# Kernel optimization log

Measured on AMD Instinct MI355X. Metric: run time of the kernel, lower is better.

Reference implementation:

```python
import jax, jax.numpy as jnp
import numpy as np

KERNEL_SIZE = 32
STRIDE = 16


def _block_compress(x, w, pe):
    # x: [B, N, H, D]; w: [K]; pe: [K, D]
    B, N, H, D = x.shape
    M = (N - KERNEL_SIZE) // STRIDE + 1
    # window gather indices: [M, K]
    idx = jnp.arange(M)[:, None] * STRIDE + jnp.arange(KERNEL_SIZE)[None, :]
    xw = x[:, idx]  # [B, M, K, H, D]
    # y = sum_k w[k] * (x_window + pe) / kernel_size
    return jnp.einsum('bmkhd,k->bmhd', xw + pe[None, None, :, None, :], w) / KERNEL_SIZE


def setup_inputs() -> dict:
    key = jax.random.key(0)
    k1, k2, k3, k4, k5, k6, k7 = jax.random.split(key, 7)
    B, N, QH, KH, D, VD = 1, 8192, 32, 2, 128, 128
    return {
        'q': jax.random.normal(k1, (B, N, QH, D), dtype=jnp.float32),
        'k': jax.random.normal(k2, (B, N, KH, D), dtype=jnp.float32),
        'v': jax.random.normal(k3, (B, N, KH, VD), dtype=jnp.float32),
        'w_key': jax.random.normal(k4, (KERNEL_SIZE,), dtype=jnp.float32),
        'pe_key': jax.random.normal(k5, (KERNEL_SIZE, D), dtype=jnp.float32),
        'w_val': jax.random.normal(k6, (KERNEL_SIZE,), dtype=jnp.float32),
        'pe_val': jax.random.normal(k7, (KERNEL_SIZE, VD), dtype=jnp.float32),
    }


def reference(q, k, v, w_key, pe_key, w_val, pe_val):
    ck = _block_compress(k, w_key, pe_key)  # [B, M, KH, D]
    cv = _block_compress(v, w_val, pe_val)  # [B, M, KH, VD]
    B, N, QH, D = q.shape
    M, KH = ck.shape[1], ck.shape[2]
    G = QH // KH  # GQA group size; off_kh = off_qh // G -> qh index = kh*G + g
    sm_scale = D ** -0.5
    qg = q.reshape(B, N, KH, G, D)
    # scores: [B, KH, G, N, M]
    scores = jnp.einsum('bnhgd,bmhd->bhgnm', qg, ck) * sm_scale
    # block-causal mask: query n attends block m iff n >= m*stride + kernel_size - 1
    n_idx = jnp.arange(N)
    m_last = jnp.arange(M) * STRIDE + KERNEL_SIZE - 1
    mask = n_idx[:, None] >= m_last[None, :]  # [N, M]
    scores = jnp.where(mask[None, None, None], scores, -jnp.inf)
    lse = jax.nn.logsumexp(scores, axis=-1)  # [B, KH, G, N]
    # queries before kernel_size-1 have no valid blocks: kernel zeros o and lse
    valid = n_idx >= KERNEL_SIZE - 1
    lse = jnp.where(valid[None, None, None], lse, 0.0)
    p = jnp.exp(scores - lse[..., None])  # exp(-inf - 0) = 0 on invalid rows
    o = jnp.einsum('bhgnm,bmhd->bnhgd', p, cv).reshape(B, N, QH, -1)
    lse = lse.reshape(B, QH, N)
    return o, lse, ck
```

## Files before the change

### kernel.cpp

```cpp
#include <hip/hip_runtime.h>

#define DI __device__ __forceinline__

using f32x4  = __attribute__((ext_vector_type(4))) float;
using bf16x8 = __attribute__((ext_vector_type(8))) short;
using u32x4  = __attribute__((ext_vector_type(4))) unsigned int;

DI unsigned short f2bf(float f) {
    unsigned int u = __float_as_uint(f);
    unsigned int r = u + 0x7FFFu + ((u >> 16) & 1u);
    return (unsigned short)(r >> 16);
}

DI void gload_lds16(const void* g, void* l) {
    __builtin_amdgcn_global_load_lds(
        (const __attribute__((address_space(1))) void*)(unsigned long long)g,
        (__attribute__((address_space(3))) void*)(unsigned int)(unsigned long long)l,
        16, 0, 0);
}

constexpr int N_SEQ = 8192;
constexpr int QH    = 32;
constexpr int KH    = 2;
constexpr int D     = 128;
constexpr int M_CMP = 511;
constexpr int MP    = 512;
constexpr int NCH   = 16;
constexpr int CHUNK_ELEMS = 16 * 64 * 8;
constexpr int HSTRIDE = NCH * CHUNK_ELEMS;

__global__ __launch_bounds__(256)
void compress_kernel(const float* __restrict__ kin, const float* __restrict__ vin,
                     const float* __restrict__ w_key, const float* __restrict__ pe_key,
                     const float* __restrict__ w_val, const float* __restrict__ pe_val,
                     float* __restrict__ ck_out,
                     unsigned short* __restrict__ kvb)
{
    const int m  = blockIdx.x;
    const int t  = threadIdx.x;
    const int hh = t >> 7;
    const int d  = t & 127;
    float acck = 0.f, accv = 0.f;
    if (m < M_CMP) {
        #pragma unroll
        for (int k = 0; k < 32; ++k) {
            float xk = kin[((m*16 + k)*KH + hh)*D + d];
            float xv = vin[((m*16 + k)*KH + hh)*D + d];
            acck += (xk + pe_key[k*D + d]) * w_key[k];
            accv += (xv + pe_val[k*D + d]) * w_val[k];
        }
        acck *= (1.f/32.f);
        accv *= (1.f/32.f);
        ck_out[(m*KH + hh)*D + d] = acck;
    }
    const int c = m >> 5, ml = m & 31;
    {
        const int mt = ml >> 4, colx = ml & 15;
        const int kc = d >> 5, hix = (d >> 3) & 3, e = d & 7;
        kvb[(size_t)hh*HSTRIDE + (((c*16 + mt*4 + kc)*64) + hix*16 + colx)*8 + e] = f2bf(acck);
    }
    {
        const int e   = ((ml >> 4) << 2) + (ml & 3);
        const int hix = (ml >> 2) & 3;
        const int dt  = d >> 4, colx = d & 15;
        kvb[(size_t)hh*HSTRIDE + (((c*16 + 8 + dt)*64) + hix*16 + colx)*8 + e] = f2bf(accv);
    }
}

__global__ __launch_bounds__(256)
void attn_kernel(const float* __restrict__ q,
                 const unsigned short* __restrict__ kvb,
                 float* __restrict__ o,
                 float* __restrict__ lse)
{
    __shared__ __align__(16) unsigned short lds[3][16][64][8];

    const int h    = blockIdx.y;
    const int bx   = (N_SEQ/8 - 1) - blockIdx.x;
    const int t    = threadIdx.x;
    const int wid  = t >> 6;
    const int lane = t & 63;
    const int col  = lane & 15;
    const int hi   = lane >> 4;

    const int n0r = (bx << 3) + (wid << 1);
    const int n1r = n0r + 1;
    const int mcnt0 = (n0r >= 31) ? (((n0r - 31) >> 4) + 1) : 0;
    const int mcnt1 = (n1r >= 31) ? (((n1r - 31) >> 4) + 1) : 0;
    const int nmax  = (bx << 3) + 7;
    const int nchb  = (nmax >= 31) ? (((((nmax - 31) >> 4) + 1) + 31) >> 5) : 0;

    const float sm_scale = 0.08838834764831845f;
    const float NEG_INF  = -__builtin_inff();

    bf16x8 qf0[4], qf1[4];
    {
        const float* qp0 = q + ((size_t)n0r*QH + (h << 4) + col)*D + (hi << 3);
        const float* qp1 = q + ((size_t)n1r*QH + (h << 4) + col)*D + (hi << 3);
        #pragma unroll
        for (int kc = 0; kc < 4; ++kc) {
            float4 a0 = *(const float4*)(qp0 + kc*32);
            float4 b0 = *(const float4*)(qp0 + kc*32 + 4);
            float4 a1 = *(const float4*)(qp1 + kc*32);
            float4 b1 = *(const float4*)(qp1 + kc*32 + 4);
            bf16x8 f0, f1;
            f0[0]=(short)f2bf(a0.x*sm_scale); f0[1]=(short)f2bf(a0.y*sm_scale);
            f0[2]=(short)f2bf(a0.z*sm_scale); f0[3]=(short)f2bf(a0.w*sm_scale);
            f0[4]=(short)f2bf(b0.x*sm_scale); f0[5]=(short)f2bf(b0.y*sm_scale);
            f0[6]=(short)f2bf(b0.z*sm_scale); f0[7]=(short)f2bf(b0.w*sm_scale);
            f1[0]=(short)f2bf(a1.x*sm_scale); f1[1]=(short)f2bf(a1.y*sm_scale);
            f1[2]=(short)f2bf(a1.z*sm_scale); f1[3]=(short)f2bf(a1.w*sm_scale);
            f1[4]=(short)f2bf(b1.x*sm_scale); f1[5]=(short)f2bf(b1.y*sm_scale);
            f1[6]=(short)f2bf(b1.z*sm_scale); f1[7]=(short)f2bf(b1.w*sm_scale);
            qf0[kc] = f0; qf1[kc] = f1;
        }
    }

    f32x4 oacc0[8], oacc1[8];
    #pragma unroll
    for (int dt = 0; dt < 8; ++dt) {
        oacc0[dt] = (f32x4){0.f,0.f,0.f,0.f};
        oacc1[dt] = (f32x4){0.f,0.f,0.f,0.f};
    }
    float rmax0 = -3e38f, rmax1 = -3e38f, rsum0 = 0.f, rsum1 = 0.f;

    const unsigned short* kvh = kvb + (size_t)h*HSTRIDE;

    auto STAGE = [&](int buf, int c) {
        const unsigned short* gp = kvh + ((size_t)(c*16 + (wid << 2))*64 + lane)*8;
        #pragma unroll
        for (int p = 0; p < 4; ++p)
            gload_lds16(gp + p*512, &lds[buf][(wid << 2) + p][lane][0]);
    };

    auto SMAX = [&](f32x4 sa, f32x4 sb, int lim, float& rm, float& rs,
                    f32x4* oaccr, unsigned int* pw) {
        float sv[8];
        if (lim < 32) {
            const int mb = hi << 2;
            #pragma unroll
            for (int jj = 0; jj < 4; ++jj) {
                sv[jj]     = (mb + jj      < lim) ? sa[jj] : NEG_INF;
                sv[4 + jj] = (mb + jj + 16 < lim) ? sb[jj] : NEG_INF;
            }
        } else {
            #pragma unroll
            for (int jj = 0; jj < 4; ++jj) { sv[jj] = sa[jj]; sv[4 + jj] = sb[jj]; }
        }
        float pm = fmaxf(fmaxf(fmaxf(sv[0],sv[1]), fmaxf(sv[2],sv[3])),
                         fmaxf(fmaxf(sv[4],sv[5]), fmaxf(sv[6],sv[7])));
        if (!__all(pm <= rm + 8.0f)) {
            float tm = pm;
            tm = fmaxf(tm, __shfl_xor(tm, 16));
            tm = fmaxf(tm, __shfl_xor(tm, 32));
            float nm = fmaxf(rm, tm);
            float sc = __expf(rm - nm);
            rs *= sc;
            #pragma unroll
            for (int dt = 0; dt < 8; ++dt) {
                oaccr[dt][0] *= sc; oaccr[dt][1] *= sc;
                oaccr[dt][2] *= sc; oaccr[dt][3] *= sc;
            }
            rm = nm;
        }
        float p[8];
        #pragma unroll
        for (int i = 0; i < 8; ++i) p[i] = __expf(sv[i] - rm);
        rs += ((p[0]+p[1]) + (p[2]+p[3])) + ((p[4]+p[5]) + (p[6]+p[7]));
        asm("v_cvt_pk_bf16_f32 %0, %1, %2" : "=v"(pw[0]) : "v"(p[0]), "v"(p[1]));
        asm("v_cvt_pk_bf16_f32 %0, %1, %2" : "=v"(pw[1]) : "v"(p[2]), "v"(p[3]));
        asm("v_cvt_pk_bf16_f32 %0, %1, %2" : "=v"(pw[2]) : "v"(p[4]), "v"(p[5]));
        asm("v_cvt_pk_bf16_f32 %0, %1, %2" : "=v"(pw[3]) : "v"(p[6]), "v"(p[7]));
    };

    if (nchb > 0) {
        STAGE(0, 0);
        STAGE(1, (1 < nchb) ? 1 : 0);

        for (int c = 0; c < nchb; ++c) {
            asm volatile("s_waitcnt vmcnt(4)" ::: "memory");
            __builtin_amdgcn_s_barrier();
            __builtin_amdgcn_sched_barrier(0);

            const int cn = (c + 2 < nchb) ? (c + 2) : (nchb - 1);
            STAGE((c + 2) % 3, cn);

            const int m0 = c << 5;
            const unsigned short (*L)[64][8] = lds[c % 3];

            f32x4 s10 = (f32x4){0,0,0,0}, s11 = (f32x4){0,0,0,0};
            f32x4 s00 = (f32x4){0,0,0,0}, s01 = (f32x4){0,0,0,0};
            __builtin_amdgcn_s_setprio(1);
            #pragma unroll
            for (int kc = 0; kc < 4; ++kc) {
                bf16x8 ca = *(const bf16x8*)&L[kc][lane][0];
                bf16x8 cb = *(const bf16x8*)&L[4 + kc][lane][0];
                s10 = __builtin_amdgcn_mfma_f32_16x16x32_bf16(ca, qf1[kc], s10, 0, 0, 0);
                s11 = __builtin_amdgcn_mfma_f32_16x16x32_bf16(cb, qf1[kc], s11, 0, 0, 0);
                s00 = __builtin_amdgcn_mfma_f32_16x16x32_bf16(ca, qf0[kc], s00, 0, 0, 0);
                s01 = __builtin_amdgcn_mfma_f32_16x16x32_bf16(cb, qf0[kc], s01, 0, 0, 0);
            }
            __builtin_amdgcn_s_setprio(0);

            unsigned int pw1[4], pw0[4];
            SMAX(s10, s11, mcnt1 - m0, rmax1, rsum1, oacc1, pw1);
            SMAX(s00, s01, mcnt0 - m0, rmax0, rsum0, oacc0, pw0);

            {
                u32x4 b1v = {pw1[0], pw1[1], pw1[2], pw1[3]};
                u32x4 b0v = {pw0[0], pw0[1], pw0[2], pw0[3]};
                __builtin_amdgcn_s_setprio(1);
                #pragma unroll
                for (int dt = 0; dt < 8; ++dt) {
                    bf16x8 cv = *(const bf16x8*)&L[8 + dt][lane][0];
                    asm("v_mfma_f32_16x16x32_bf16 %0, %1, %2, %0"
                        : "+v"(oacc1[dt]) : "v"(cv), "v"(b1v));
                    asm("v_mfma_f32_16x16x32_bf16 %0, %1, %2, %0"
                        : "+v"(oacc0[dt]) : "v"(cv), "v"(b0v));
                }
                __builtin_amdgcn_s_setprio(0);
            }
        }
    }

    auto EPI = [&](int n, float rm, float rs, f32x4* oaccr, bool valid) {
        float r = rs;
        r += __shfl_xor(r, 16);
        r += __shfl_xor(r, 32);
        const float inv = valid ? (1.0f / r) : 0.0f;
        float* op = o + ((size_t)n*QH + (h << 4) + col)*D + (hi << 2);
        #pragma unroll
        for (int dt = 0; dt < 8; ++dt) {
            f32x4 w = oaccr[dt];
            w[0] *= inv; w[1] *= inv; w[2] *= inv; w[3] *= inv;
            *(f32x4*)(op + dt*16) = w;
        }
        if (lane < 16) {
            float lv = valid ? (rm + __logf(r)) : 0.0f;
            lse[((size_t)(h << 4) + col)*N_SEQ + n] = lv;
        }
    };
    EPI(n0r, rmax0, rsum0, oacc0, mcnt0 > 0);
    EPI(n1r, rmax1, rsum1, oacc1, mcnt1 > 0);
}

extern "C" void kernel_launch(void* const* d_in, const int* in_sizes, int n_in,
                              void* d_out, int out_size, void* d_ws, size_t ws_size,
                              hipStream_t stream)
{
    const float* q      = (const float*)d_in[0];
    const float* k      = (const float*)d_in[1];
    const float* v      = (const float*)d_in[2];
    const float* w_key  = (const float*)d_in[3];
    const float* pe_key = (const float*)d_in[4];
    const float* w_val  = (const float*)d_in[5];
    const float* pe_val = (const float*)d_in[6];

    float* o   = (float*)d_out;
    float* lse = o + (size_t)N_SEQ * QH * D;
    float* ck  = lse + (size_t)QH * N_SEQ;

    unsigned short* kvb = (unsigned short*)d_ws;

    compress_kernel<<<dim3(MP), dim3(256), 0, stream>>>(
        k, v, w_key, pe_key, w_val, pe_val, ck, kvb);

    attn_kernel<<<dim3(N_SEQ/8, KH), dim3(256), 0, stream>>>(
        q, kvb, o, lse);
}
```

Before: 93.59 us.

## Process four query rows per wave to double KV reuse per staged chunk

Each workgroup now covers 16 query positions instead of 8, with each wave handling four rows in two pairs, so every compressed K/V chunk staged into LDS is reused by twice as many queries. The grid halves and global and LDS traffic per query drops. In exchange, register pressure grows (query fragments and output accumulators double), launch bounds now request 2 waves per SIMD, and there are fewer workgroups to balance the causal triangle.

Measured after the change: 96.76 us. +3.4%, slower.

```diff
diff --git a/kernel.cpp b/kernel.cpp
--- a/kernel.cpp
+++ b/kernel.cpp
@@ -67,7 +67,7 @@
     }
 }
 
-__global__ __launch_bounds__(256)
+__global__ __launch_bounds__(256, 2)
 void attn_kernel(const float* __restrict__ q,
                  const unsigned short* __restrict__ kvb,
                  float* __restrict__ o,
@@ -76,53 +76,51 @@
     __shared__ __align__(16) unsigned short lds[3][16][64][8];
 
     const int h    = blockIdx.y;
-    const int bx   = (N_SEQ/8 - 1) - blockIdx.x;
+    const int bx   = (N_SEQ/16 - 1) - blockIdx.x;
     const int t    = threadIdx.x;
     const int wid  = t >> 6;
     const int lane = t & 63;
     const int col  = lane & 15;
     const int hi   = lane >> 4;
 
-    const int n0r = (bx << 3) + (wid << 1);
-    const int n1r = n0r + 1;
-    const int mcnt0 = (n0r >= 31) ? (((n0r - 31) >> 4) + 1) : 0;
-    const int mcnt1 = (n1r >= 31) ? (((n1r - 31) >> 4) + 1) : 0;
-    const int nmax  = (bx << 3) + 7;
-    const int nchb  = (nmax >= 31) ? (((((nmax - 31) >> 4) + 1) + 31) >> 5) : 0;
+    const int nbase = (bx << 4) + (wid << 2);
+    int mcnt[4];
+    #pragma unroll
+    for (int r = 0; r < 4; ++r) {
+        const int nr = nbase + r;
+        mcnt[r] = (nr >= 31) ? (((nr - 31) >> 4) + 1) : 0;
+    }
+    const int nmax = (bx << 4) + 15;
+    const int nchb = (nmax >= 31) ? (((((nmax - 31) >> 4) + 1) + 31) >> 5) : 0;
 
     const float sm_scale = 0.08838834764831845f;
     const float NEG_INF  = -__builtin_inff();
 
-    bf16x8 qf0[4], qf1[4];
-    {
-        const float* qp0 = q + ((size_t)n0r*QH + (h << 4) + col)*D + (hi << 3);
-        const float* qp1 = q + ((size_t)n1r*QH + (h << 4) + col)*D + (hi << 3);
+    bf16x8 qf[4][4];
+    #pragma unroll
+    for (int r = 0; r < 4; ++r) {
+        const float* qp = q + ((size_t)(nbase + r)*QH + (h << 4) + col)*D + (hi << 3);
         #pragma unroll
         for (int kc = 0; kc < 4; ++kc) {
-            float4 a0 = *(const float4*)(qp0 + kc*32);
-            float4 b0 = *(const float4*)(qp0 + kc*32 + 4);
-            float4 a1 = *(const float4*)(qp1 + kc*32);
-            float4 b1 = *(const float4*)(qp1 + kc*32 + 4);
-            bf16x8 f0, f1;
-            f0[0]=(short)f2bf(a0.x*sm_scale); f0[1]=(short)f2bf(a0.y*sm_scale);
-            f0[2]=(short)f2bf(a0.z*sm_scale); f0[3]=(short)f2bf(a0.w*sm_scale);
-            f0[4]=(short)f2bf(b0.x*sm_scale); f0[5]=(short)f2bf(b0.y*sm_scale);
-            f0[6]=(short)f2bf(b0.z*sm_scale); f0[7]=(short)f2bf(b0.w*sm_scale);
-            f1[0]=(short)f2bf(a1.x*sm_scale); f1[1]=(short)f2bf(a1.y*sm_scale);
-            f1[2]=(short)f2bf(a1.z*sm_scale); f1[3]=(short)f2bf(a1.w*sm_scale);
-            f1[4]=(short)f2bf(b1.x*sm_scale); f1[5]=(short)f2bf(b1.y*sm_scale);
-            f1[6]=(short)f2bf(b1.z*sm_scale); f1[7]=(short)f2bf(b1.w*sm_scale);
-            qf0[kc] = f0; qf1[kc] = f1;
-        }
-    }
-
-    f32x4 oacc0[8], oacc1[8];
-    #pragma unroll
-    for (int dt = 0; dt < 8; ++dt) {
-        oacc0[dt] = (f32x4){0.f,0.f,0.f,0.f};
-        oacc1[dt] = (f32x4){0.f,0.f,0.f,0.f};
-    }
-    float rmax0 = -3e38f, rmax1 = -3e38f, rsum0 = 0.f, rsum1 = 0.f;
+            f32x4 a = *(const f32x4*)(qp + kc*32);
+            f32x4 b = *(const f32x4*)(qp + kc*32 + 4);
+            bf16x8 f;
+            f[0]=(short)f2bf(a[0]*sm_scale); f[1]=(short)f2bf(a[1]*sm_scale);
+            f[2]=(short)f2bf(a[2]*sm_scale); f[3]=(short)f2bf(a[3]*sm_scale);
+            f[4]=(short)f2bf(b[0]*sm_scale); f[5]=(short)f2bf(b[1]*sm_scale);
+            f[6]=(short)f2bf(b[2]*sm_scale); f[7]=(short)f2bf(b[3]*sm_scale);
+            qf[r][kc] = f;
+        }
+    }
+
+    f32x4 oacc[4][8];
+    #pragma unroll
+    for (int r = 0; r < 4; ++r)
+        #pragma unroll
+        for (int dt = 0; dt < 8; ++dt)
+            oacc[r][dt] = (f32x4){0.f,0.f,0.f,0.f};
+    float rmax[4] = {-3e38f,-3e38f,-3e38f,-3e38f};
+    float rsum[4] = {0.f,0.f,0.f,0.f};
 
     const unsigned short* kvh = kvb + (size_t)h*HSTRIDE;
 
@@ -188,60 +186,64 @@
             const int m0 = c << 5;
             const unsigned short (*L)[64][8] = lds[c % 3];
 
-            f32x4 s10 = (f32x4){0,0,0,0}, s11 = (f32x4){0,0,0,0};
-            f32x4 s00 = (f32x4){0,0,0,0}, s01 = (f32x4){0,0,0,0};
-            __builtin_amdgcn_s_setprio(1);
-            #pragma unroll
-            for (int kc = 0; kc < 4; ++kc) {
-                bf16x8 ca = *(const bf16x8*)&L[kc][lane][0];
-                bf16x8 cb = *(const bf16x8*)&L[4 + kc][lane][0];
-                s10 = __builtin_amdgcn_mfma_f32_16x16x32_bf16(ca, qf1[kc], s10, 0, 0, 0);
-                s11 = __builtin_amdgcn_mfma_f32_16x16x32_bf16(cb, qf1[kc], s11, 0, 0, 0);
-                s00 = __builtin_amdgcn_mfma_f32_16x16x32_bf16(ca, qf0[kc], s00, 0, 0, 0);
-                s01 = __builtin_amdgcn_mfma_f32_16x16x32_bf16(cb, qf0[kc], s01, 0, 0, 0);
-            }
-            __builtin_amdgcn_s_setprio(0);
-
-            unsigned int pw1[4], pw0[4];
-            SMAX(s10, s11, mcnt1 - m0, rmax1, rsum1, oacc1, pw1);
-            SMAX(s00, s01, mcnt0 - m0, rmax0, rsum0, oacc0, pw0);
-
-            {
-                u32x4 b1v = {pw1[0], pw1[1], pw1[2], pw1[3]};
-                u32x4 b0v = {pw0[0], pw0[1], pw0[2], pw0[3]};
+            #pragma unroll
+            for (int pr = 0; pr < 2; ++pr) {
+                const int r0 = pr*2, r1 = pr*2 + 1;
+
+                f32x4 sA0 = (f32x4){0,0,0,0}, sA1 = (f32x4){0,0,0,0};
+                f32x4 sB0 = (f32x4){0,0,0,0}, sB1 = (f32x4){0,0,0,0};
+                __builtin_amdgcn_s_setprio(1);
+                #pragma unroll
+                for (int kc = 0; kc < 4; ++kc) {
+                    bf16x8 ca = *(const bf16x8*)&L[kc][lane][0];
+                    bf16x8 cb = *(const bf16x8*)&L[4 + kc][lane][0];
+                    sA0 = __builtin_amdgcn_mfma_f32_16x16x32_bf16(ca, qf[r0][kc], sA0, 0, 0, 0);
+                    sA1 = __builtin_amdgcn_mfma_f32_16x16x32_bf16(cb, qf[r0][kc], sA1, 0, 0, 0);
+                    sB0 = __builtin_amdgcn_mfma_f32_16x16x32_bf16(ca, qf[r1][kc], sB0, 0, 0, 0);
+                    sB1 = __builtin_amdgcn_mfma_f32_16x16x32_bf16(cb, qf[r1][kc], sB1, 0, 0, 0);
+                }
+                __builtin_amdgcn_s_setprio(0);
+
+                unsigned int pwA[4], pwB[4];
+                SMAX(sA0, sA1, mcnt[r0] - m0, rmax[r0], rsum[r0], oacc[r0], pwA);
+                SMAX(sB0, sB1, mcnt[r1] - m0, rmax[r1], rsum[r1], oacc[r1], pwB);
+
+                u32x4 bAv = {pwA[0], pwA[1], pwA[2], pwA[3]};
+                u32x4 bBv = {pwB[0], pwB[1], pwB[2], pwB[3]};
                 __builtin_amdgcn_s_setprio(1);
                 #pragma unroll
                 for (int dt = 0; dt < 8; ++dt) {
                     bf16x8 cv = *(const bf16x8*)&L[8 + dt][lane][0];
                     asm("v_mfma_f32_16x16x32_bf16 %0, %1, %2, %0"
-                        : "+v"(oacc1[dt]) : "v"(cv), "v"(b1v));
+                        : "+v"(oacc[r0][dt]) : "v"(cv), "v"(bAv));
                     asm("v_mfma_f32_16x16x32_bf16 %0, %1, %2, %0"
-                        : "+v"(oacc0[dt]) : "v"(cv), "v"(b0v));
+                        : "+v"(oacc[r1][dt]) : "v"(cv), "v"(bBv));
                 }
                 __builtin_amdgcn_s_setprio(0);
             }
         }
     }
 
-    auto EPI = [&](int n, float rm, float rs, f32x4* oaccr, bool valid) {
-        float r = rs;
-        r += __shfl_xor(r, 16);
-        r += __shfl_xor(r, 32);
-        const float inv = valid ? (1.0f / r) : 0.0f;
+    #pragma unroll
+    for (int r = 0; r < 4; ++r) {
+        const int n = nbase + r;
+        float rr = rsum[r];
+        rr += __shfl_xor(rr, 16);
+        rr += __shfl_xor(rr, 32);
+        const bool valid = mcnt[r] > 0;
+        const float inv = valid ? (1.0f / rr) : 0.0f;
         float* op = o + ((size_t)n*QH + (h << 4) + col)*D + (hi << 2);
         #pragma unroll
         for (int dt = 0; dt < 8; ++dt) {
-            f32x4 w = oaccr[dt];
+            f32x4 w = oacc[r][dt];
             w[0] *= inv; w[1] *= inv; w[2] *= inv; w[3] *= inv;
             *(f32x4*)(op + dt*16) = w;
         }
         if (lane < 16) {
-            float lv = valid ? (rm + __logf(r)) : 0.0f;
+            float lv = valid ? (rmax[r] + __logf(rr)) : 0.0f;
             lse[((size_t)(h << 4) + col)*N_SEQ + n] = lv;
         }
-    };
-    EPI(n0r, rmax0, rsum0, oacc0, mcnt0 > 0);
-    EPI(n1r, rmax1, rsum1, oacc1, mcnt1 > 0);
+    }
 }
 
 extern "C" void kernel_launch(void* const* d_in, const int* in_sizes, int n_in,
@@ -265,6 +267,6 @@
     compress_kernel<<<dim3(MP), dim3(256), 0, stream>>>(
         k, v, w_key, pe_key, w_val, pe_val, ck, kvb);
 
-    attn_kernel<<<dim3(N_SEQ/8, KH), dim3(256), 0, stream>>>(
+    attn_kernel<<<dim3(N_SEQ/16, KH), dim3(256), 0, stream>>>(
         q, kvb, o, lse);
 }
```
